# Optimization experiments

Measured on AMD Instinct MI355X. Metric: run time of the kernel, lower is better.

The kernel has to match this reference:

```python
import jax, jax.numpy as jnp
import numpy as np

N_NODES = 50000
N_EDGES = 800000
HIDDEN = 256
LAYERS = 10


def setup_inputs() -> dict:
    key = jax.random.key(0)
    ks = jax.random.split(key, 8)
    x = jax.random.normal(ks[0], (N_NODES, 1), dtype=jnp.float32)
    edge_index = jax.random.randint(ks[1], (2, N_EDGES), 0, N_NODES, dtype=jnp.int64)
    # GCNConv weights (Glorot-ish scale)
    W1 = jax.random.normal(ks[2], (1, HIDDEN), dtype=jnp.float32) * (1.0 / np.sqrt(1))
    b1 = jnp.zeros((HIDDEN,), dtype=jnp.float32)
    W = jax.random.normal(ks[3], (HIDDEN, HIDDEN), dtype=jnp.float32) * (1.0 / np.sqrt(HIDDEN))
    b = jnp.zeros((HIDDEN,), dtype=jnp.float32)
    Wc = jax.random.normal(ks[4], (HIDDEN, 1), dtype=jnp.float32) * (1.0 / np.sqrt(HIDDEN))
    bc = jnp.zeros((1,), dtype=jnp.float32)
    return {"x": x, "edge_index": edge_index, "W1": W1, "b1": b1,
            "W": W, "b": b, "Wc": Wc, "bc": bc}


def _gcn_norm(edge_index, n_nodes):
    # PyG GCNConv default: add self-loops, symmetric normalization
    loop = jnp.arange(n_nodes, dtype=edge_index.dtype)
    src = jnp.concatenate([edge_index[0], loop])
    dst = jnp.concatenate([edge_index[1], loop])
    ones = jnp.ones(src.shape[0], dtype=jnp.float32)
    deg = jax.ops.segment_sum(ones, dst, num_segments=n_nodes)
    dinv = jnp.where(deg > 0, jax.lax.rsqrt(deg), 0.0)
    norm = dinv[src] * dinv[dst]  # [E+N]
    return src, dst, norm


def _gcn_conv(h, W, b, src, dst, norm, n_nodes):
    h = h @ W                                   # [N, H] dense transform first (small GEMM)
    msg = h[src] * norm[:, None]                # gather + scale  [E+N, H]
    out = jax.ops.segment_sum(msg, dst, num_segments=n_nodes)  # scatter-add
    return out + b


def reference(x, edge_index, W1, b1, W, b, Wc, bc):
    n = x.shape[0]
    src, dst, norm = _gcn_norm(edge_index, n)  # graph is static across layers
    h = jax.nn.relu(_gcn_conv(x, W1, b1, src, dst, norm, n))
    for _ in range(1, LAYERS):  # layers 1..9 share the same weights (self.conv reused)
        h = jax.nn.relu(_gcn_conv(h, W, b, src, dst, norm, n))
    return h @ Wc + bc  # [N, 1]
```

## Files before the change

### kernel.cpp

```cpp
#include <hip/hip_runtime.h>

typedef long long ll;
typedef __attribute__((ext_vector_type(8))) short short8;
typedef __attribute__((ext_vector_type(4))) float f32x4;
constexpr int HID = 256;
constexpr int LDSS = 264;

__device__ inline ushort f2bf(float f){
  uint u = __float_as_uint(f);
  u += 0x7FFFu + ((u >> 16) & 1u);
  return (ushort)(u >> 16);
}

__global__ void k_diag(float* out, int n, float val){
  int i = blockIdx.x*256 + threadIdx.x;
  if (i < n) out[i] = val;
}

__global__ void k_detect(const int* ei, int* flag){
  __shared__ int bad;
  if (threadIdx.x == 0) bad = 0;
  __syncthreads();
  for (int i = threadIdx.x; i < 2048; i += 256)
    if (ei[2*i+1] != 0) bad = 1;
  __syncthreads();
  if (threadIdx.x == 0) *flag = bad ? 0 : 1;
}

__global__ void k_count(const int* ei, ll E, const int* flag, int* cnt){
  ll i = (ll)blockIdx.x*256 + threadIdx.x;
  if (i >= E) return;
  int f = *flag;
  int d = f ? (int)((const ll*)ei)[E + i] : ei[E + i];
  atomicAdd(&cnt[d], 1);
}

__global__ void k_scan_a(const int* __restrict__ cnt, int* __restrict__ bsum, int n){
  __shared__ int s[256];
  int t = threadIdx.x, i = blockIdx.x*256 + t;
  s[t] = (i < n) ? cnt[i] : 0;
  __syncthreads();
  for (int off = 128; off; off >>= 1){
    if (t < off) s[t] += s[t + off];
    __syncthreads();
  }
  if (t == 0) bsum[blockIdx.x] = s[0];
}

__global__ void k_scan_b(const int* __restrict__ bsum, int* __restrict__ boff,
                         int nb, int* __restrict__ row_ptr, int n){
  __shared__ int s[256];
  int t = threadIdx.x;
  int v = (t < nb) ? bsum[t] : 0;
  s[t] = v; __syncthreads();
  for (int off = 1; off < 256; off <<= 1){
    int add = (t >= off) ? s[t - off] : 0;
    __syncthreads();
    s[t] += add;
    __syncthreads();
  }
  if (t < nb) boff[t] = s[t] - v;
  if (t == nb - 1) row_ptr[n] = s[t];
}

__global__ void k_scan_c(const int* __restrict__ cnt, const int* __restrict__ boff,
                         int* __restrict__ row_ptr, int n){
  __shared__ int s[256];
  int t = threadIdx.x, i = blockIdx.x*256 + t;
  int v = (i < n) ? cnt[i] : 0;
  s[t] = v; __syncthreads();
  for (int off = 1; off < 256; off <<= 1){
    int add = (t >= off) ? s[t - off] : 0;
    __syncthreads();
    s[t] += add;
    __syncthreads();
  }
  if (i < n) row_ptr[i] = boff[blockIdx.x] + s[t] - v;
}

__global__ void k_dinv(const int* cnt, const float* x, float* dinv, float* xd, int n){
  int i = blockIdx.x*256 + threadIdx.x;
  if (i >= n) return;
  float dv = 1.0f / sqrtf((float)(cnt[i] + 1));
  dinv[i] = dv;
  xd[i] = x[i] * dv;
}

__global__ void k_place(const int* ei, ll E, const int* flag, int* fill, int* col){
  ll i = (ll)blockIdx.x*256 + threadIdx.x;
  if (i >= E) return;
  int f = *flag;
  int s, d;
  if (f){ const ll* e64 = (const ll*)ei; s = (int)e64[i]; d = (int)e64[E + i]; }
  else  { s = ei[i]; d = ei[E + i]; }
  int p = atomicAdd(&fill[d], 1);
  col[p] = s;
}

__global__ void k_layer1(const float* __restrict__ xd, const int* __restrict__ row_ptr,
                         const int* __restrict__ col, float* __restrict__ g, int n){
  int i = blockIdx.x*256 + threadIdx.x;
  if (i >= n) return;
  float s = xd[i];
  int e0 = row_ptr[i], e1 = row_ptr[i+1];
  for (int e = e0; e < e1; ++e) s += xd[col[e]];
  g[i] = s;
}

__global__ void k_splitW(const float* __restrict__ W, short* __restrict__ Bt){
  int idx = blockIdx.x*256 + threadIdx.x;
  if (idx >= 16*8*64) return;
  int nb = idx >> 9, kc = (idx >> 6) & 7, l = idx & 63;
  short8 hi, lo;
  #pragma unroll
  for (int j = 0; j < 8; ++j){
    int k = kc*32 + ((l >> 4) * 8) + j;
    int c = nb*16 + (l & 15);
    float wv = W[k*HID + c];
    ushort h = f2bf(wv);
    float hf = __uint_as_float((uint)h << 16);
    hi[j] = (short)h;
    lo[j] = (short)f2bf(wv - hf);
  }
  ((short8*)Bt)[idx] = hi;
  ((short8*)Bt)[8192 + idx] = lo;
}

template<int MODE>
__global__ __launch_bounds__(256, 4) void k_gemm_mfma(
  const void* __restrict__ Ain, const short* __restrict__ Bt,
  const float* __restrict__ bias, const float* __restrict__ W1,
  const float* __restrict__ dinv, ushort* __restrict__ ts_bf, int n)
{
  __shared__ short Ah[64*LDSS];
  int t = threadIdx.x;
  int r0 = blockIdx.x * 64;

  #pragma unroll
  for (int i = 0; i < 8; ++i){
    int id  = i*256 + t;
    int row = id >> 5;
    int c16 = id & 31;
    int v   = r0 + row;
    short8 hi8 = {0,0,0,0,0,0,0,0};
    if (v < n){
      if (MODE == 0){
        float gv = dinv[v] * ((const float*)Ain)[v];
        const float4* wp = (const float4*)(W1 + c16*8);
        const float4* bp = (const float4*)(bias + c16*8);
        float4 w0 = wp[0], w1 = wp[1], b0 = bp[0], b1 = bp[1];
        hi8[0] = (short)f2bf(fmaxf(fmaf(gv,w0.x,b0.x), 0.f));
        hi8[1] = (short)f2bf(fmaxf(fmaf(gv,w0.y,b0.y), 0.f));
        hi8[2] = (short)f2bf(fmaxf(fmaf(gv,w0.z,b0.z), 0.f));
        hi8[3] = (short)f2bf(fmaxf(fmaf(gv,w0.w,b0.w), 0.f));
        hi8[4] = (short)f2bf(fmaxf(fmaf(gv,w1.x,b1.x), 0.f));
        hi8[5] = (short)f2bf(fmaxf(fmaf(gv,w1.y,b1.y), 0.f));
        hi8[6] = (short)f2bf(fmaxf(fmaf(gv,w1.z,b1.z), 0.f));
        hi8[7] = (short)f2bf(fmaxf(fmaf(gv,w1.w,b1.w), 0.f));
      } else {
        hi8 = ((const short8*)Ain)[(size_t)v*32 + c16];
      }
    }
    *(short8*)&Ah[row*LDSS + c16*8] = hi8;
  }
  __syncthreads();

  int l = t & 63, w = t >> 6;
  const short8* Btv = (const short8*)Bt;
  f32x4 acc[4][4];
  #pragma unroll
  for (int m = 0; m < 4; ++m)
    #pragma unroll
    for (int nf = 0; nf < 4; ++nf)
      acc[m][nf] = (f32x4){0.f,0.f,0.f,0.f};

  for (int kc = 0; kc < 8; ++kc){
    short8 ah[4];
    #pragma unroll
    for (int m = 0; m < 4; ++m){
      int row = m*16 + (l & 15);
      ah[m] = *(const short8*)&Ah[row*LDSS + (kc*4 + (l >> 4))*8];
    }
    #pragma unroll
    for (int nf = 0; nf < 4; ++nf){
      int nb = w*4 + nf;
      short8 bh = Btv[(size_t)(nb*8 + kc)*64 + l];
      short8 bl = Btv[(size_t)8192 + (nb*8 + kc)*64 + l];
      #pragma unroll
      for (int m = 0; m < 4; ++m){
        acc[m][nf] = __builtin_amdgcn_mfma_f32_16x16x32_bf16(ah[m], bh, acc[m][nf], 0,0,0);
        acc[m][nf] = __builtin_amdgcn_mfma_f32_16x16x32_bf16(ah[m], bl, acc[m][nf], 0,0,0);
      }
    }
  }

  #pragma unroll
  for (int m = 0; m < 4; ++m){
    int rowb = r0 + m*16 + ((l >> 4)*4);
    #pragma unroll
    for (int r = 0; r < 4; ++r){
      int v = rowb + r;
      if (v < n){
        float dv = dinv[v];
        #pragma unroll
        for (int nf = 0; nf < 4; ++nf){
          int colb = w*64 + nf*16 + (l & 15);
          ts_bf[(size_t)v*HID + colb] = f2bf(dv * acc[m][nf][r]);
        }
      }
    }
  }
}

__device__ inline void bfacc(uint2 u, float4& a){
  a.x += __uint_as_float(u.x << 16);
  a.y += __uint_as_float(u.x & 0xFFFF0000u);
  a.z += __uint_as_float(u.y << 16);
  a.w += __uint_as_float(u.y & 0xFFFF0000u);
}

template<int LAST>
__global__ __launch_bounds__(256, 4) void k_scatter_bf(
  const ushort* __restrict__ ts_bf, const int* __restrict__ row_ptr,
  const int* __restrict__ col, const float* __restrict__ bias,
  const float* __restrict__ dinv, ushort* __restrict__ Abf,
  const float* __restrict__ Wc, const float* __restrict__ bc,
  float* __restrict__ out, int n)
{
  int w = (int)((blockIdx.x*256 + threadIdx.x) >> 6);
  int lane = threadIdx.x & 63;
  if (w >= n) return;
  const uint2* tsp = ((const uint2*)ts_bf) + lane;
  int e0 = row_ptr[w], e1 = row_ptr[w+1];

  float4 a0 = make_float4(0.f,0.f,0.f,0.f);
  float4 a1 = make_float4(0.f,0.f,0.f,0.f);
  float4 a2 = make_float4(0.f,0.f,0.f,0.f);
  float4 a3 = make_float4(0.f,0.f,0.f,0.f);
  bfacc(tsp[(size_t)w*64], a0);

  int e = e0;
  for (; e + 8 <= e1; e += 8){
    int c[8];
    #pragma unroll
    for (int j = 0; j < 8; ++j) c[j] = __builtin_nontemporal_load(col + e + j);
    uint2 v[8];
    #pragma unroll
    for (int j = 0; j < 8; ++j) v[j] = tsp[(size_t)c[j]*64];
    bfacc(v[0], a0); bfacc(v[1], a1); bfacc(v[2], a2); bfacc(v[3], a3);
    bfacc(v[4], a0); bfacc(v[5], a1); bfacc(v[6], a2); bfacc(v[7], a3);
  }
  for (; e + 2 <= e1; e += 2){
    int c0 = __builtin_nontemporal_load(col + e);
    int c1 = __builtin_nontemporal_load(col + e + 1);
    uint2 v0 = tsp[(size_t)c0*64];
    uint2 v1 = tsp[(size_t)c1*64];
    bfacc(v0, a0); bfacc(v1, a1);
  }
  if (e < e1){
    uint2 v = tsp[(size_t)__builtin_nontemporal_load(col + e)*64];
    bfacc(v, a0);
  }

  a0.x += a1.x + a2.x + a3.x;
  a0.y += a1.y + a2.y + a3.y;
  a0.z += a1.z + a2.z + a3.z;
  a0.w += a1.w + a2.w + a3.w;

  float dv = dinv[w];
  float4 bb = ((const float4*)bias)[lane];
  if (LAST == 0){
    uint2 o;
    o.x = (uint)f2bf(fmaxf(fmaf(dv, a0.x, bb.x), 0.f))
        | ((uint)f2bf(fmaxf(fmaf(dv, a0.y, bb.y), 0.f)) << 16);
    o.y = (uint)f2bf(fmaxf(fmaf(dv, a0.z, bb.z), 0.f))
        | ((uint)f2bf(fmaxf(fmaf(dv, a0.w, bb.w), 0.f)) << 16);
    ((uint2*)Abf)[(size_t)w*64 + lane] = o;
  } else {
    float4 wc = ((const float4*)Wc)[lane];
    float s = fmaxf(fmaf(dv, a0.x, bb.x), 0.f)*wc.x
            + fmaxf(fmaf(dv, a0.y, bb.y), 0.f)*wc.y
            + fmaxf(fmaf(dv, a0.z, bb.z), 0.f)*wc.z
            + fmaxf(fmaf(dv, a0.w, bb.w), 0.f)*wc.w;
    #pragma unroll
    for (int off = 32; off; off >>= 1) s += __shfl_down(s, off, 64);
    if (lane == 0) out[w] = s + bc[0];
  }
}

extern "C" void kernel_launch(void* const* d_in, const int* in_sizes, int n_in,
                              void* d_out, int out_size, void* d_ws, size_t ws_size,
                              hipStream_t stream)
{
  const float* x  = (const float*)d_in[0];
  const int*   ei = (const int*)d_in[1];
  const float* W1 = (const float*)d_in[2];
  const float* b1 = (const float*)d_in[3];
  const float* Wm = (const float*)d_in[4];
  const float* bm = (const float*)d_in[5];
  const float* Wc = (const float*)d_in[6];
  const float* bc = (const float*)d_in[7];
  float* out = (float*)d_out;
  const int N = in_sizes[0];
  const ll  E = in_sizes[1] / 2;

  char* ws = (char*)d_ws;
  size_t off = 0;
  auto carve = [&](size_t bytes)->char*{
    char* p = ws + off; off += (bytes + 255) & ~(size_t)255; return p;
  };
  int*   cnt     = (int*)  carve((size_t)N*4);
  int*   row_ptr = (int*)  carve((size_t)(N+1)*4);
  int*   fill    = (int*)  carve((size_t)N*4);
  float* dinv    = (float*)carve((size_t)N*4);
  float* xd      = (float*)carve((size_t)N*4);
  float* g       = (float*)carve((size_t)N*4);
  int*   flag    = (int*)  carve(256);
  int*   bsum    = (int*)  carve(1024);
  int*   boff    = (int*)  carve(1024);
  short* Bt      = (short*)carve((size_t)2*8192*8*2);
  int*   col     = (int*)  carve((size_t)E*4);
  ushort* ts_bf  = (ushort*)carve((size_t)N*HID*2);
  ushort* Abf    = (ushort*)carve((size_t)N*HID*2);
  if (off > ws_size){
    k_diag<<<(out_size+255)/256, 256, 0, stream>>>(out, out_size, (float)(ws_size >> 20));
    return;
  }

  hipMemsetAsync(cnt, 0, (size_t)N*4, stream);
  k_detect<<<1, 256, 0, stream>>>(ei, flag);
  int eblocks = (int)((E + 255) / 256);
  k_count<<<eblocks, 256, 0, stream>>>(ei, E, flag, cnt);
  int nb = (N + 255) / 256;
  k_scan_a<<<nb, 256, 0, stream>>>(cnt, bsum, N);
  k_scan_b<<<1, 256, 0, stream>>>(bsum, boff, nb, row_ptr, N);
  k_scan_c<<<nb, 256, 0, stream>>>(cnt, boff, row_ptr, N);
  k_dinv<<<(N+255)/256, 256, 0, stream>>>(cnt, x, dinv, xd, N);
  hipMemcpyAsync(fill, row_ptr, (size_t)N*4, hipMemcpyDeviceToDevice, stream);
  k_place<<<eblocks, 256, 0, stream>>>(ei, E, flag, fill, col);
  k_splitW<<<32, 256, 0, stream>>>(Wm, Bt);
  k_layer1<<<(N+255)/256, 256, 0, stream>>>(xd, row_ptr, col, g, N);

  int gblocks = (N + 63) / 64;
  int sblocks = (N + 3) / 4;
  k_gemm_mfma<0><<<gblocks, 256, 0, stream>>>(g, Bt, b1, W1, dinv, ts_bf, N);
  k_scatter_bf<0><<<sblocks, 256, 0, stream>>>(ts_bf, row_ptr, col, bm, dinv, Abf, Wc, bc, out, N);
  for (int l = 0; l < 7; ++l){
    k_gemm_mfma<1><<<gblocks, 256, 0, stream>>>(Abf, Bt, bm, nullptr, dinv, ts_bf, N);
    k_scatter_bf<0><<<sblocks, 256, 0, stream>>>(ts_bf, row_ptr, col, bm, dinv, Abf, Wc, bc, out, N);
  }
  k_gemm_mfma<1><<<gblocks, 256, 0, stream>>>(Abf, Bt, bm, nullptr, dinv, ts_bf, N);
  k_scatter_bf<1><<<sblocks, 256, 0, stream>>>(ts_bf, row_ptr, col, bm, dinv, Abf, Wc, bc, out, N);
}
```

Baseline: 869.1 us.

## Permute hidden-channel layout so GEMM epilogue writes packed 8-byte stores

Introduces a fixed permutation of the hidden dimension so each GEMM lane can pack its four accumulator columns into one uint2 store instead of four scattered 2-byte stores. The weight split, biases, layer-1 weights and classifier weights are permuted to match, so the stored activations stay in the permuted order through all layers. It also folds the dinv computation into the scan kernel to remove one launch, and shrinks the scatter gather unroll from 8 to 4. This adds a small permutation kernel, and the smaller unroll lowers memory-level parallelism in the gather loop.

```diff
diff --git a/kernel.cpp b/kernel.cpp
--- a/kernel.cpp
+++ b/kernel.cpp
@@ -11,6 +11,8 @@
   u += 0x7FFFu + ((u >> 16) & 1u);
   return (ushort)(u >> 16);
 }
+
+__device__ inline int pinv(int q){ return (q & ~63) | ((q & 3)*16 + ((q >> 2) & 15)); }
 
 __global__ void k_diag(float* out, int n, float val){
   int i = blockIdx.x*256 + threadIdx.x;
@@ -64,7 +66,8 @@
 }
 
 __global__ void k_scan_c(const int* __restrict__ cnt, const int* __restrict__ boff,
-                         int* __restrict__ row_ptr, int n){
+                         int* __restrict__ row_ptr, const float* __restrict__ x,
+                         float* __restrict__ dinv, float* __restrict__ xd, int n){
   __shared__ int s[256];
   int t = threadIdx.x, i = blockIdx.x*256 + t;
   int v = (i < n) ? cnt[i] : 0;
@@ -75,15 +78,12 @@
     s[t] += add;
     __syncthreads();
   }
-  if (i < n) row_ptr[i] = boff[blockIdx.x] + s[t] - v;
-}
-
-__global__ void k_dinv(const int* cnt, const float* x, float* dinv, float* xd, int n){
-  int i = blockIdx.x*256 + threadIdx.x;
-  if (i >= n) return;
-  float dv = 1.0f / sqrtf((float)(cnt[i] + 1));
-  dinv[i] = dv;
-  xd[i] = x[i] * dv;
+  if (i < n){
+    row_ptr[i] = boff[blockIdx.x] + s[t] - v;
+    float dv = 1.0f / sqrtf((float)(v + 1));
+    dinv[i] = dv;
+    xd[i] = x[i] * dv;
+  }
 }
 
 __global__ void k_place(const int* ei, ll E, const int* flag, int* fill, int* col){
@@ -107,6 +107,16 @@
   g[i] = s;
 }
 
+__global__ void k_perm(const float* b1, const float* W1, const float* bm, const float* Wc,
+                       float* b1_p, float* W1_p, float* bm_p, float* Wc_p){
+  int q = threadIdx.x;
+  int c = pinv(q);
+  b1_p[q] = b1[c];
+  W1_p[q] = W1[c];
+  bm_p[q] = bm[c];
+  Wc_p[q] = Wc[c];
+}
+
 __global__ void k_splitW(const float* __restrict__ W, short* __restrict__ Bt){
   int idx = blockIdx.x*256 + threadIdx.x;
   if (idx >= 16*8*64) return;
@@ -114,7 +124,7 @@
   short8 hi, lo;
   #pragma unroll
   for (int j = 0; j < 8; ++j){
-    int k = kc*32 + ((l >> 4) * 8) + j;
+    int k = pinv(kc*32 + ((l >> 4) * 8) + j);
     int c = nb*16 + (l & 15);
     float wv = W[k*HID + c];
     ushort h = f2bf(wv);
@@ -196,17 +206,15 @@
 
   #pragma unroll
   for (int m = 0; m < 4; ++m){
-    int rowb = r0 + m*16 + ((l >> 4)*4);
     #pragma unroll
     for (int r = 0; r < 4; ++r){
-      int v = rowb + r;
+      int v = r0 + m*16 + ((l >> 4)*4) + r;
       if (v < n){
         float dv = dinv[v];
-        #pragma unroll
-        for (int nf = 0; nf < 4; ++nf){
-          int colb = w*64 + nf*16 + (l & 15);
-          ts_bf[(size_t)v*HID + colb] = f2bf(dv * acc[m][nf][r]);
-        }
+        uint2 o;
+        o.x = (uint)f2bf(dv * acc[m][0][r]) | ((uint)f2bf(dv * acc[m][1][r]) << 16);
+        o.y = (uint)f2bf(dv * acc[m][2][r]) | ((uint)f2bf(dv * acc[m][3][r]) << 16);
+        *(uint2*)((char*)ts_bf + (size_t)v*512 + w*128 + (l & 15)*8) = o;
       }
     }
   }
@@ -240,24 +248,18 @@
   bfacc(tsp[(size_t)w*64], a0);
 
   int e = e0;
-  for (; e + 8 <= e1; e += 8){
-    int c[8];
-    #pragma unroll
-    for (int j = 0; j < 8; ++j) c[j] = __builtin_nontemporal_load(col + e + j);
-    uint2 v[8];
-    #pragma unroll
-    for (int j = 0; j < 8; ++j) v[j] = tsp[(size_t)c[j]*64];
-    bfacc(v[0], a0); bfacc(v[1], a1); bfacc(v[2], a2); bfacc(v[3], a3);
-    bfacc(v[4], a0); bfacc(v[5], a1); bfacc(v[6], a2); bfacc(v[7], a3);
-  }
-  for (; e + 2 <= e1; e += 2){
-    int c0 = __builtin_nontemporal_load(col + e);
+  for (; e + 4 <= e1; e += 4){
+    int c0 = __builtin_nontemporal_load(col + e + 0);
     int c1 = __builtin_nontemporal_load(col + e + 1);
+    int c2 = __builtin_nontemporal_load(col + e + 2);
+    int c3 = __builtin_nontemporal_load(col + e + 3);
     uint2 v0 = tsp[(size_t)c0*64];
     uint2 v1 = tsp[(size_t)c1*64];
-    bfacc(v0, a0); bfacc(v1, a1);
-  }
-  if (e < e1){
+    uint2 v2 = tsp[(size_t)c2*64];
+    uint2 v3 = tsp[(size_t)c3*64];
+    bfacc(v0, a0); bfacc(v1, a1); bfacc(v2, a2); bfacc(v3, a3);
+  }
+  for (; e < e1; ++e){
     uint2 v = tsp[(size_t)__builtin_nontemporal_load(col + e)*64];
     bfacc(v, a0);
   }
@@ -318,6 +320,10 @@
   int*   flag    = (int*)  carve(256);
   int*   bsum    = (int*)  carve(1024);
   int*   boff    = (int*)  carve(1024);
+  float* b1_p    = (float*)carve(1024);
+  float* W1_p    = (float*)carve(1024);
+  float* bm_p    = (float*)carve(1024);
+  float* Wc_p    = (float*)carve(1024);
   short* Bt      = (short*)carve((size_t)2*8192*8*2);
   int*   col     = (int*)  carve((size_t)E*4);
   ushort* ts_bf  = (ushort*)carve((size_t)N*HID*2);
@@ -334,21 +340,21 @@
   int nb = (N + 255) / 256;
   k_scan_a<<<nb, 256, 0, stream>>>(cnt, bsum, N);
   k_scan_b<<<1, 256, 0, stream>>>(bsum, boff, nb, row_ptr, N);
-  k_scan_c<<<nb, 256, 0, stream>>>(cnt, boff, row_ptr, N);
-  k_dinv<<<(N+255)/256, 256, 0, stream>>>(cnt, x, dinv, xd, N);
+  k_scan_c<<<nb, 256, 0, stream>>>(cnt, boff, row_ptr, x, dinv, xd, N);
   hipMemcpyAsync(fill, row_ptr, (size_t)N*4, hipMemcpyDeviceToDevice, stream);
   k_place<<<eblocks, 256, 0, stream>>>(ei, E, flag, fill, col);
+  k_perm<<<1, 256, 0, stream>>>(b1, W1, bm, Wc, b1_p, W1_p, bm_p, Wc_p);
   k_splitW<<<32, 256, 0, stream>>>(Wm, Bt);
   k_layer1<<<(N+255)/256, 256, 0, stream>>>(xd, row_ptr, col, g, N);
 
   int gblocks = (N + 63) / 64;
   int sblocks = (N + 3) / 4;
-  k_gemm_mfma<0><<<gblocks, 256, 0, stream>>>(g, Bt, b1, W1, dinv, ts_bf, N);
-  k_scatter_bf<0><<<sblocks, 256, 0, stream>>>(ts_bf, row_ptr, col, bm, dinv, Abf, Wc, bc, out, N);
+  k_gemm_mfma<0><<<gblocks, 256, 0, stream>>>(g, Bt, b1_p, W1_p, dinv, ts_bf, N);
+  k_scatter_bf<0><<<sblocks, 256, 0, stream>>>(ts_bf, row_ptr, col, bm_p, dinv, Abf, Wc_p, bc, out, N);
   for (int l = 0; l < 7; ++l){
-    k_gemm_mfma<1><<<gblocks, 256, 0, stream>>>(Abf, Bt, bm, nullptr, dinv, ts_bf, N);
-    k_scatter_bf<0><<<sblocks, 256, 0, stream>>>(ts_bf, row_ptr, col, bm, dinv, Abf, Wc, bc, out, N);
-  }
-  k_gemm_mfma<1><<<gblocks, 256, 0, stream>>>(Abf, Bt, bm, nullptr, dinv, ts_bf, N);
-  k_scatter_bf<1><<<sblocks, 256, 0, stream>>>(ts_bf, row_ptr, col, bm, dinv, Abf, Wc, bc, out, N);
-}
+    k_gemm_mfma<1><<<gblocks, 256, 0, stream>>>(Abf, Bt, bm_p, nullptr, dinv, ts_bf, N);
+    k_scatter_bf<0><<<sblocks, 256, 0, stream>>>(ts_bf, row_ptr, col, bm_p, dinv, Abf, Wc_p, bc, out, N);
+  }
+  k_gemm_mfma<1><<<gblocks, 256, 0, stream>>>(Abf, Bt, bm_p, nullptr, dinv, ts_bf, N);
+  k_scatter_bf<1><<<sblocks, 256, 0, stream>>>(ts_bf, row_ptr, col, bm_p, dinv, Abf, Wc_p, bc, out, N);
+}
```

New measurement: 876.7 us. Within noise of the previous version (+0.9%).
